# Optimization experiments

Measured on AMD Instinct MI355X. Metric: run time of the kernel, lower is better.

The kernel has to match this reference:

```python
import jax, jax.numpy as jnp
import numpy as np
import math

N = 50000      # nodes (single node type 'mapping_var')
D = 128        # in_feats
R = 3          # relations
E = 800000     # edges per relation
OUT = 64
ALPHA = 0.5
BETA1 = math.log(2.0)    # log(lambda/layer + 1), layer=1, lambda=1
BETA2 = math.log(1.5)    # layer=2
SLOPE = 0.01             # leaky_relu default negative slope


def setup_inputs() -> dict:
    key = jax.random.key(0)
    ks = jax.random.split(key, 8)
    x = jax.random.normal(ks[0], (N, D), dtype=jnp.float32)
    src = jax.random.randint(ks[1], (R, E), 0, N, dtype=jnp.int32)
    dst = jax.random.randint(ks[2], (R, E), 0, N, dtype=jnp.int32)
    W1 = jax.random.normal(ks[3], (R, D, D), dtype=jnp.float32) * 0.05
    b1 = jnp.zeros((R, D), dtype=jnp.float32)
    W2 = jax.random.normal(ks[4], (R, D, D), dtype=jnp.float32) * 0.05
    b2 = jnp.zeros((R, D), dtype=jnp.float32)
    Wlin = jax.random.normal(ks[5], (D, OUT), dtype=jnp.float32) * 0.05
    blin = jnp.zeros((OUT,), dtype=jnp.float32)
    return {"x": x, "src": src, "dst": dst, "W1": W1, "b1": b1,
            "W2": W2, "b2": b2, "Wlin": Wlin, "blin": blin}


def _gcn2_rel(h, feat0, src, dst, W, b, beta, act):
    """One GCN2Conv on one relation. h,feat0: [N,D]; src,dst: [E]."""
    ones = jnp.ones(src.shape, h.dtype)
    deg_out = jnp.maximum(jax.ops.segment_sum(ones, src, num_segments=N), 1.0)
    deg_in = jnp.maximum(jax.ops.segment_sum(ones, dst, num_segments=N), 1.0)
    hs = h * (deg_out ** -0.5)[:, None]              # src-side normalize
    agg = jax.ops.segment_sum(hs[src], dst, num_segments=N)  # SpMM via gather+scatter
    feat = agg * (deg_in ** -0.5)[:, None]           # dst-side normalize
    rst = feat * (1.0 - ALPHA) + ALPHA * feat0       # initial-residual blend
    rst = (1.0 - beta) * rst + beta * (rst @ W) + b  # identity mapping (project_initial_features)
    if act:
        rst = jnp.where(rst >= 0, rst, SLOPE * rst)  # leaky_relu
    return rst


def reference(x, src, dst, W1, b1, W2, b2, Wlin, blin):
    # conv1: per-relation GCN2Conv(layer=1, leaky_relu), mean-aggregate over relations
    h1 = jax.vmap(lambda s, d, w, bb: _gcn2_rel(x, x, s, d, w, bb, BETA1, True))(
        src, dst, W1, b1).mean(axis=0)
    # dropout: eval-mode identity
    # conv2: per-relation GCN2Conv(layer=2, no activation), feat_0 = original inputs
    h2 = jax.vmap(lambda s, d, w, bb: _gcn2_rel(h1, x, s, d, w, bb, BETA2, False))(
        src, dst, W2, b2).mean(axis=0)
    return h2 @ Wlin + blin
```

## Files before the change

### kernel.cpp

```cpp
#include <hip/hip_runtime.h>

#define NN    50000
#define DD    128
#define RR    3
#define EE    800000
#define OUTD  64
#define BKT   128
#define NBK   391
#define CAP   2560
#define CAPB  2560
#define CHUNK 2048
#define NCH   391
#define NPB   3125
#define SETUPB 6250
#define ALPHA_ 0.5f
#define SLOPE_ 0.01f
#define BETA1_ 0.6931471805599453f
#define BETA2_ 0.4054651081081644f

typedef __attribute__((ext_vector_type(8))) short short8;
typedef __attribute__((ext_vector_type(4))) float f32x4;

__device__ __forceinline__ unsigned short f2b(float f) {
    unsigned int u = __builtin_bit_cast(unsigned int, f);
    u += 0x7FFFu + ((u >> 16) & 1u);
    return (unsigned short)(u >> 16);
}
__device__ __forceinline__ unsigned int pack2(float lo, float hi) {
    return (unsigned int)f2b(lo) | ((unsigned int)f2b(hi) << 16);
}
__device__ __forceinline__ float blo(unsigned int w) { return __builtin_bit_cast(float, w << 16); }
__device__ __forceinline__ float bhi(unsigned int w) { return __builtin_bit_cast(float, w & 0xFFFF0000u); }

__global__ __launch_bounds__(256) void bin_kernel(
    const int* __restrict__ src, const int* __restrict__ dst,
    int* __restrict__ bcnt_d, int* __restrict__ bcnt_s,
    int* __restrict__ pairs_d, unsigned short* __restrict__ pairs_s)
{
    __shared__ int hist[NBK];
    __shared__ int lbase[NBK];
    __shared__ int gdelta[NBK];
    __shared__ int lcur[NBK];
    __shared__ unsigned int staging[CHUNK];
    unsigned short* staging16 = (unsigned short*)staging;
    const int tid = threadIdx.x;
    const int blk = blockIdx.x;
    const int phase = (blk >= RR * NCH);
    const int rb = phase ? blk - RR * NCH : blk;
    const int r = rb / NCH;
    const int chunk = rb % NCH;
    const int e0 = chunk * CHUNK;
    const int n = min(CHUNK, EE - e0);
    const int* sp = src + (size_t)r * EE + e0;
    const int* dp = dst + (size_t)r * EE + e0;
    const int* kp = phase ? sp : dp;

    for (int i = tid; i < NBK; i += 256) hist[i] = 0;
    __syncthreads();
    for (int i = tid; i < n; i += 256)
        atomicAdd(&hist[kp[i] >> 7], 1);
    __syncthreads();
    if (tid < 64) {
        int carry = 0;
        for (int c0 = 0; c0 < NBK; c0 += 64) {
            const int idx = c0 + tid;
            const int v = (idx < NBK) ? hist[idx] : 0;
            int incl = v;
            #pragma unroll
            for (int d = 1; d < 64; d <<= 1) {
                const int t = __shfl_up(incl, d, 64);
                if (tid >= d) incl += t;
            }
            if (idx < NBK) lbase[idx] = carry + incl - v;
            carry += __shfl(incl, 63, 64);
        }
    }
    __syncthreads();
    if (!phase) {
        for (int b = tid; b < NBK; b += 256) {
            lcur[b] = lbase[b];
            const int h = hist[b];
            if (h > 0) {
                const int gstart = (r * NBK + b) * CAP + atomicAdd(&bcnt_d[r * NBK + b], h);
                gdelta[b] = gstart - lbase[b];
            }
        }
        __syncthreads();
        for (int i = tid; i < n; i += 256) {
            const int d = dp[i];
            const int b = d >> 7;
            const int pos = atomicAdd(&lcur[b], 1);
            staging[pos] = (unsigned int)sp[i] | ((unsigned int)(d & 127) << 16)
                         | ((unsigned int)b << 23);
        }
        __syncthreads();
        for (int j = tid; j < n; j += 256) {
            const unsigned int v = staging[j];
            const int b = v >> 23;
            const int gi = gdelta[b] + j;
            const int lo = gi - (r * NBK + b) * CAP;
            if (lo < CAP) pairs_d[gi] = (int)(v & 0x7FFFFF);
        }
    } else {
        for (int b = tid; b < NBK; b += 256) {
            lcur[b] = lbase[b];
            const int h = hist[b];
            if (h > 0) {
                const int gstart = (r * NBK + b) * CAPB + atomicAdd(&bcnt_s[r * NBK + b], h);
                gdelta[b] = gstart - lbase[b];
            }
        }
        __syncthreads();
        for (int i = tid; i < n; i += 256) {
            const int s = sp[i];
            const int b = s >> 7;
            const int pos = atomicAdd(&lcur[b], 1);
            staging16[pos] = (unsigned short)((b << 7) | (s & 127));
        }
        __syncthreads();
        for (int j = tid; j < n; j += 256) {
            const unsigned short v = staging16[j];
            const int b = v >> 7;
            const int gi = gdelta[b] + j;
            const int lo = gi - (r * NBK + b) * CAPB;
            if (lo < CAPB) pairs_s[gi] = v;
        }
    }
}

__global__ __launch_bounds__(256) void dego_setup_kernel(
    const unsigned short* __restrict__ pairs_s, const int* __restrict__ bcnt_s,
    float* __restrict__ dego_r,
    const float* __restrict__ x, unsigned short* __restrict__ xb,
    const float* __restrict__ W1, const float* __restrict__ W2,
    const float* __restrict__ Wlin, unsigned short* __restrict__ Wt1,
    unsigned short* __restrict__ Wt2, unsigned short* __restrict__ WlT)
{
    __shared__ int scnt[BKT];
    const int tid = threadIdx.x;
    const int blk = blockIdx.x;
    if (blk < RR * NBK) {
        const int n2 = min(bcnt_s[blk], CAPB);
        const unsigned short* ps = pairs_s + (size_t)blk * CAPB;
        if (tid < BKT) scnt[tid] = 0;
        __syncthreads();
        for (int i = tid; i < n2; i += 256)
            atomicAdd(&scnt[ps[i] & 127], 1);
        __syncthreads();
        if (tid < BKT) {
            const int r = blk / NBK;
            const int g = (blk % NBK) * BKT + tid;
            if (g < NN)
                dego_r[r * NN + g] = rsqrtf((float)max(scnt[tid], 1));
        }
    } else {
        const int i = (blk - RR * NBK) * 256 + tid;
        {
            const float4 v = ((const float4*)x)[i];
            ushort4 o;
            o.x = f2b(v.x); o.y = f2b(v.y); o.z = f2b(v.z); o.w = f2b(v.w);
            ((ushort4*)xb)[i] = o;
        }
        if (i < RR * DD * DD) {
            const int r = i >> 14, rem = i & 16383, nn = rem >> 7, k = rem & 127;
            const float diag = (k == nn) ? 1.0f : 0.0f;
            const float w1 = W1[r * DD * DD + k * DD + nn];
            Wt1[i] = f2b(BETA1_ * w1 + diag * (1.0f - BETA1_));
            const float w2 = W2[r * DD * DD + k * DD + nn];
            Wt2[i] = f2b((BETA2_ * w2 + diag * (1.0f - BETA2_)) * (1.0f / 3.0f));
        } else if (i < RR * DD * DD + OUTD * DD) {
            const int j = i - RR * DD * DD;
            const int nn = j >> 7, k = j & 127;
            WlT[j] = f2b(Wlin[k * OUTD + nn]);
        }
    }
}

__global__ __launch_bounds__(256) void sort_kernel(
    int* __restrict__ pairs_d, const int* __restrict__ bcnt_d,
    const float* __restrict__ dego_r,
    int* __restrict__ off_g, int* __restrict__ cnt_g, float* __restrict__ degi_r)
{
    __shared__ int stage[CAP];
    __shared__ int cnt[BKT];
    __shared__ int base[BKT];
    __shared__ int pos[BKT];
    const int tid = threadIdx.x;
    const int bid = blockIdx.x;
    const int rr = bid / NBK;
    const int n = min(bcnt_d[bid], CAP);
    int* pp = pairs_d + (size_t)bid * CAP;
    const float* dego = dego_r + (size_t)rr * NN;
    if (tid < BKT) cnt[tid] = 0;
    __syncthreads();
    for (int i = tid; i < n; i += 256) {
        const int p = pp[i];
        stage[i] = p;
        atomicAdd(&cnt[p >> 16], 1);
    }
    __syncthreads();
    if (tid < 64) {
        int carry = 0;
        for (int c0 = 0; c0 < BKT; c0 += 64) {
            const int v = cnt[c0 + tid];
            int incl = v;
            #pragma unroll
            for (int d = 1; d < 64; d <<= 1) {
                const int t = __shfl_up(incl, d, 64);
                if (tid >= d) incl += t;
            }
            base[c0 + tid] = carry + incl - v;
            carry += __shfl(incl, 63, 64);
        }
    }
    __syncthreads();
    if (tid < BKT) {
        pos[tid] = base[tid];
        const int g = (bid % NBK) * BKT + tid;
        if (g < NN) {
            off_g[rr * NN + g] = bid * CAP + base[tid];
            cnt_g[rr * NN + g] = cnt[tid];
            degi_r[rr * NN + g] = rsqrtf((float)max(cnt[tid], 1));
        }
    }
    __syncthreads();
    for (int i = tid; i < n; i += 256) {
        const int p = stage[i];
        const int q = atomicAdd(&pos[p >> 16], 1);
        const int s = p & 0xFFFF;
        pp[q] = s | ((int)f2b(dego[s]) << 16);
    }
}

__global__ __launch_bounds__(256) void pull_all_kernel(
    const unsigned short* __restrict__ hb,
    const unsigned short* __restrict__ xb,
    const int* __restrict__ csrw, const int* __restrict__ off_g,
    const int* __restrict__ cnt_g, const float* __restrict__ degi_r,
    unsigned short* __restrict__ aggb)
{
    const int blk = blockIdx.x;
    const int r = blk / NPB;
    const int node = (blk % NPB) * 16 + (threadIdx.x >> 4);
    const int lane = threadIdx.x & 15;
    const int gi = r * NN + node;
    const int j0 = off_g[gi];
    const int j1 = j0 + cnt_g[gi];
    const uint4* hb4 = (const uint4*)hb;
    float a0 = 0.f, a1 = 0.f, a2 = 0.f, a3 = 0.f, a4 = 0.f, a5 = 0.f, a6 = 0.f, a7 = 0.f;
    int j = j0;
    for (; j + 4 <= j1; j += 4) {
        const unsigned int p0 = csrw[j],     p1 = csrw[j + 1];
        const unsigned int p2 = csrw[j + 2], p3 = csrw[j + 3];
        const float n0 = bhi(p0), n1 = bhi(p1), n2 = bhi(p2), n3 = bhi(p3);
        const uint4 q0 = hb4[(size_t)(p0 & 0xFFFF) * 16 + lane];
        const uint4 q1 = hb4[(size_t)(p1 & 0xFFFF) * 16 + lane];
        const uint4 q2 = hb4[(size_t)(p2 & 0xFFFF) * 16 + lane];
        const uint4 q3 = hb4[(size_t)(p3 & 0xFFFF) * 16 + lane];
        a0 += blo(q0.x) * n0 + blo(q1.x) * n1 + blo(q2.x) * n2 + blo(q3.x) * n3;
        a1 += bhi(q0.x) * n0 + bhi(q1.x) * n1 + bhi(q2.x) * n2 + bhi(q3.x) * n3;
        a2 += blo(q0.y) * n0 + blo(q1.y) * n1 + blo(q2.y) * n2 + blo(q3.y) * n3;
        a3 += bhi(q0.y) * n0 + bhi(q1.y) * n1 + bhi(q2.y) * n2 + bhi(q3.y) * n3;
        a4 += blo(q0.z) * n0 + blo(q1.z) * n1 + blo(q2.z) * n2 + blo(q3.z) * n3;
        a5 += bhi(q0.z) * n0 + bhi(q1.z) * n1 + bhi(q2.z) * n2 + bhi(q3.z) * n3;
        a6 += blo(q0.w) * n0 + blo(q1.w) * n1 + blo(q2.w) * n2 + blo(q3.w) * n3;
        a7 += bhi(q0.w) * n0 + bhi(q1.w) * n1 + bhi(q2.w) * n2 + bhi(q3.w) * n3;
    }
    for (; j < j1; ++j) {
        const unsigned int p0 = csrw[j];
        const float n0 = bhi(p0);
        const uint4 q0 = hb4[(size_t)(p0 & 0xFFFF) * 16 + lane];
        a0 += blo(q0.x) * n0; a1 += bhi(q0.x) * n0;
        a2 += blo(q0.y) * n0; a3 += bhi(q0.y) * n0;
        a4 += blo(q0.z) * n0; a5 += bhi(q0.z) * n0;
        a6 += blo(q0.w) * n0; a7 += bhi(q0.w) * n0;
    }
    const float nd = degi_r[gi] * (1.0f - ALPHA_);
    const uint4 xq = ((const uint4*)xb)[(size_t)node * 16 + lane];
    uint4 o;
    o.x = pack2(a0 * nd + ALPHA_ * blo(xq.x), a1 * nd + ALPHA_ * bhi(xq.x));
    o.y = pack2(a2 * nd + ALPHA_ * blo(xq.y), a3 * nd + ALPHA_ * bhi(xq.y));
    o.z = pack2(a4 * nd + ALPHA_ * blo(xq.z), a5 * nd + ALPHA_ * bhi(xq.z));
    o.w = pack2(a6 * nd + ALPHA_ * blo(xq.w), a7 * nd + ALPHA_ * bhi(xq.w));
    ((uint4*)aggb)[(size_t)gi * 16 + lane] = o;
}

template<int LIN>
__global__ __launch_bounds__(256) void conv_mfma_kernel(
    const unsigned short* __restrict__ aggb,
    const unsigned short* __restrict__ WtG,
    const float* __restrict__ bias,
    const unsigned short* __restrict__ WlT,
    const float* __restrict__ blin,
    unsigned short* __restrict__ houtb,
    float* __restrict__ outf)
{
    __shared__ unsigned short WtL[DD * 136];
    uint4* WtL4 = (uint4*)WtL;
    const int tid  = threadIdx.x;
    const int wave = tid >> 6;
    const int lane = tid & 63;
    const int l15  = lane & 15;
    const int q    = lane >> 4;
    const int blockRow = blockIdx.x * 64;
    const int row0 = blockRow + wave * 16;
    const int arow = min(row0 + l15, NN - 1);

    f32x4 o[8];
    if (LIN) {
        #pragma unroll
        for (int ct = 0; ct < 8; ++ct) {
            const int col = ct * 16 + l15;
            const float bv = (bias[col] + bias[DD + col] + bias[2 * DD + col]) * (1.0f / 3.0f);
            o[ct] = (f32x4){bv, bv, bv, bv};
        }
    } else {
        #pragma unroll
        for (int ct = 0; ct < 8; ++ct) o[ct] = (f32x4){0.f, 0.f, 0.f, 0.f};
    }

    for (int r = 0; r < RR; ++r) {
        __syncthreads();
        const uint4* wg = (const uint4*)(WtG + (size_t)r * DD * DD);
        for (int i = tid; i < DD * 16; i += 256)
            WtL4[(i >> 4) * 17 + (i & 15)] = wg[i];
        __syncthreads();

        short8 a[4];
        const uint4* ap = (const uint4*)aggb + ((size_t)r * NN + arow) * 16 + q;
        #pragma unroll
        for (int ks = 0; ks < 4; ++ks)
            a[ks] = __builtin_bit_cast(short8, ap[ks * 4]);

        #pragma unroll
        for (int ct = 0; ct < 8; ++ct) {
            f32x4 acc;
            if (LIN) {
                acc = o[ct];
            } else {
                const float bv = bias[r * DD + ct * 16 + l15];
                acc = (f32x4){bv, bv, bv, bv};
            }
            const int nrow = ct * 16 + l15;
            #pragma unroll
            for (int ks = 0; ks < 4; ++ks) {
                const short8 b = __builtin_bit_cast(short8, WtL4[nrow * 17 + ks * 4 + q]);
                acc = __builtin_amdgcn_mfma_f32_16x16x32_bf16(a[ks], b, acc, 0, 0, 0);
            }
            if (LIN) {
                o[ct] = acc;
            } else {
                #pragma unroll
                for (int e = 0; e < 4; ++e) {
                    float v = acc[e];
                    v = v >= 0.f ? v : SLOPE_ * v;
                    o[ct][e] += v * (1.0f / 3.0f);
                }
            }
        }
    }

    __syncthreads();
    unsigned short* tile = WtL;
    #pragma unroll
    for (int ct = 0; ct < 8; ++ct) {
        const int col = ct * 16 + l15;
        #pragma unroll
        for (int e = 0; e < 4; ++e) {
            const int lrow = wave * 16 + q * 4 + e;
            tile[lrow * 136 + col] = f2b(o[ct][e]);
        }
    }
    if (LIN) {
        uint4* wl4 = WtL4 + 64 * 17;
        const uint4* wg = (const uint4*)WlT;
        for (int i = tid; i < OUTD * 16; i += 256)
            wl4[(i >> 4) * 17 + (i & 15)] = wg[i];
    }
    __syncthreads();

    if (!LIN) {
        for (int i = tid; i < 64 * 16; i += 256) {
            const int lrow = i >> 4, c = i & 15;
            const int grow = blockRow + lrow;
            if (grow < NN)
                ((uint4*)houtb)[(size_t)grow * 16 + c] = WtL4[lrow * 17 + c];
        }
    } else {
        short8 a2[4];
        const int lrow = wave * 16 + l15;
        #pragma unroll
        for (int ks = 0; ks < 4; ++ks)
            a2[ks] = __builtin_bit_cast(short8, WtL4[lrow * 17 + ks * 4 + q]);
        #pragma unroll
        for (int ct = 0; ct < 4; ++ct) {
            const int col = ct * 16 + l15;
            const float bv = blin[col];
            f32x4 acc = (f32x4){bv, bv, bv, bv};
            #pragma unroll
            for (int ks = 0; ks < 4; ++ks) {
                const short8 b = __builtin_bit_cast(short8, WtL4[(64 + col) * 17 + ks * 4 + q]);
                acc = __builtin_amdgcn_mfma_f32_16x16x32_bf16(a2[ks], b, acc, 0, 0, 0);
            }
            #pragma unroll
            for (int e = 0; e < 4; ++e) {
                const int grow = row0 + q * 4 + e;
                if (grow < NN) outf[(size_t)grow * OUTD + col] = acc[e];
            }
        }
    }
}

extern "C" void kernel_launch(void* const* d_in, const int* in_sizes, int n_in,
                              void* d_out, int out_size, void* d_ws, size_t ws_size,
                              hipStream_t stream)
{
    const float* x    = (const float*)d_in[0];
    const int*   src  = (const int*)  d_in[1];
    const int*   dst  = (const int*)  d_in[2];
    const float* W1   = (const float*)d_in[3];
    const float* b1   = (const float*)d_in[4];
    const float* W2   = (const float*)d_in[5];
    const float* b2   = (const float*)d_in[6];
    const float* Wlin = (const float*)d_in[7];
    const float* blin = (const float*)d_in[8];
    float* out = (float*)d_out;

    int*   bcnt_d  = (int*)d_ws;
    int*   bcnt_s  = bcnt_d + RR * NBK;
    float* dego_r  = (float*)(bcnt_s + RR * NBK);
    float* degi_r  = dego_r + RR * NN;
    int*   off_g   = (int*)(degi_r + RR * NN);
    int*   cnt_g   = off_g + RR * NN;
    int*   pairs_d = cnt_g + RR * NN + 2;
    unsigned short* pairs_s = (unsigned short*)(pairs_d + (size_t)RR * NBK * CAP);
    unsigned short* xb   = pairs_s + (size_t)RR * NBK * CAPB;
    unsigned short* h1b  = xb + (size_t)NN * DD;
    unsigned short* aggb = h1b + (size_t)NN * DD;
    unsigned short* Wt1  = aggb + (size_t)RR * NN * DD;
    unsigned short* Wt2  = Wt1 + RR * DD * DD;
    unsigned short* WlT  = Wt2 + RR * DD * DD;

    hipMemsetAsync(bcnt_d, 0, (size_t)2 * RR * NBK * sizeof(int), stream);

    const int gemm_blocks = (NN + 63) / 64;

    bin_kernel<<<2 * RR * NCH, 256, 0, stream>>>(src, dst, bcnt_d, bcnt_s, pairs_d, pairs_s);
    dego_setup_kernel<<<RR * NBK + SETUPB, 256, 0, stream>>>(
        pairs_s, bcnt_s, dego_r, x, xb, W1, W2, Wlin, Wt1, Wt2, WlT);
    sort_kernel<<<RR * NBK, 256, 0, stream>>>(
        pairs_d, bcnt_d, dego_r, off_g, cnt_g, degi_r);

    pull_all_kernel<<<RR * NPB, 256, 0, stream>>>(
        xb, xb, pairs_d, off_g, cnt_g, degi_r, aggb);
    conv_mfma_kernel<0><<<gemm_blocks, 256, 0, stream>>>(
        aggb, Wt1, b1, nullptr, nullptr, h1b, nullptr);

    pull_all_kernel<<<RR * NPB, 256, 0, stream>>>(
        h1b, xb, pairs_d, off_g, cnt_g, degi_r, aggb);
    conv_mfma_kernel<1><<<gemm_blocks, 256, 0, stream>>>(
        aggb, Wt2, b2, WlT, blin, nullptr, out);
}
```

Before: 415.5 us.

## Fuse neighbor gather-aggregation into the MFMA conv kernel, eliminating the aggb intermediate

Replaces the separate pull (SpMM gather) kernel and the MFMA GEMM kernel with one fused kernel. Each lane gathers its 64-byte slice of neighbor rows and applies the degree scaling and residual blend in registers, then packs the result straight into MFMA A fragments. This removes the write and re-read of the 3×N×D bf16 aggregation buffer and two kernel launches per layer. In exchange, the irregular gather runs with far fewer threads: 782 blocks, 4 lanes per row, and relations processed one after another. That may expose memory latency and lower occupancy for what was a latency-bound gather.

New measurement: 457.9 us. 10.2% more time.

```diff
diff --git a/kernel.cpp b/kernel.cpp
--- a/kernel.cpp
+++ b/kernel.cpp
@@ -11,7 +11,6 @@
 #define CAPB  2560
 #define CHUNK 2048
 #define NCH   391
-#define NPB   3125
 #define SETUPB 6250
 #define ALPHA_ 0.5f
 #define SLOPE_ 0.01f
@@ -232,62 +231,12 @@
     }
 }
 
-__global__ __launch_bounds__(256) void pull_all_kernel(
+template<int LIN>
+__global__ __launch_bounds__(256, 4) void fused_conv_kernel(
     const unsigned short* __restrict__ hb,
     const unsigned short* __restrict__ xb,
     const int* __restrict__ csrw, const int* __restrict__ off_g,
     const int* __restrict__ cnt_g, const float* __restrict__ degi_r,
-    unsigned short* __restrict__ aggb)
-{
-    const int blk = blockIdx.x;
-    const int r = blk / NPB;
-    const int node = (blk % NPB) * 16 + (threadIdx.x >> 4);
-    const int lane = threadIdx.x & 15;
-    const int gi = r * NN + node;
-    const int j0 = off_g[gi];
-    const int j1 = j0 + cnt_g[gi];
-    const uint4* hb4 = (const uint4*)hb;
-    float a0 = 0.f, a1 = 0.f, a2 = 0.f, a3 = 0.f, a4 = 0.f, a5 = 0.f, a6 = 0.f, a7 = 0.f;
-    int j = j0;
-    for (; j + 4 <= j1; j += 4) {
-        const unsigned int p0 = csrw[j],     p1 = csrw[j + 1];
-        const unsigned int p2 = csrw[j + 2], p3 = csrw[j + 3];
-        const float n0 = bhi(p0), n1 = bhi(p1), n2 = bhi(p2), n3 = bhi(p3);
-        const uint4 q0 = hb4[(size_t)(p0 & 0xFFFF) * 16 + lane];
-        const uint4 q1 = hb4[(size_t)(p1 & 0xFFFF) * 16 + lane];
-        const uint4 q2 = hb4[(size_t)(p2 & 0xFFFF) * 16 + lane];
-        const uint4 q3 = hb4[(size_t)(p3 & 0xFFFF) * 16 + lane];
-        a0 += blo(q0.x) * n0 + blo(q1.x) * n1 + blo(q2.x) * n2 + blo(q3.x) * n3;
-        a1 += bhi(q0.x) * n0 + bhi(q1.x) * n1 + bhi(q2.x) * n2 + bhi(q3.x) * n3;
-        a2 += blo(q0.y) * n0 + blo(q1.y) * n1 + blo(q2.y) * n2 + blo(q3.y) * n3;
-        a3 += bhi(q0.y) * n0 + bhi(q1.y) * n1 + bhi(q2.y) * n2 + bhi(q3.y) * n3;
-        a4 += blo(q0.z) * n0 + blo(q1.z) * n1 + blo(q2.z) * n2 + blo(q3.z) * n3;
-        a5 += bhi(q0.z) * n0 + bhi(q1.z) * n1 + bhi(q2.z) * n2 + bhi(q3.z) * n3;
-        a6 += blo(q0.w) * n0 + blo(q1.w) * n1 + blo(q2.w) * n2 + blo(q3.w) * n3;
-        a7 += bhi(q0.w) * n0 + bhi(q1.w) * n1 + bhi(q2.w) * n2 + bhi(q3.w) * n3;
-    }
-    for (; j < j1; ++j) {
-        const unsigned int p0 = csrw[j];
-        const float n0 = bhi(p0);
-        const uint4 q0 = hb4[(size_t)(p0 & 0xFFFF) * 16 + lane];
-        a0 += blo(q0.x) * n0; a1 += bhi(q0.x) * n0;
-        a2 += blo(q0.y) * n0; a3 += bhi(q0.y) * n0;
-        a4 += blo(q0.z) * n0; a5 += bhi(q0.z) * n0;
-        a6 += blo(q0.w) * n0; a7 += bhi(q0.w) * n0;
-    }
-    const float nd = degi_r[gi] * (1.0f - ALPHA_);
-    const uint4 xq = ((const uint4*)xb)[(size_t)node * 16 + lane];
-    uint4 o;
-    o.x = pack2(a0 * nd + ALPHA_ * blo(xq.x), a1 * nd + ALPHA_ * bhi(xq.x));
-    o.y = pack2(a2 * nd + ALPHA_ * blo(xq.y), a3 * nd + ALPHA_ * bhi(xq.y));
-    o.z = pack2(a4 * nd + ALPHA_ * blo(xq.z), a5 * nd + ALPHA_ * bhi(xq.z));
-    o.w = pack2(a6 * nd + ALPHA_ * blo(xq.w), a7 * nd + ALPHA_ * bhi(xq.w));
-    ((uint4*)aggb)[(size_t)gi * 16 + lane] = o;
-}
-
-template<int LIN>
-__global__ __launch_bounds__(256) void conv_mfma_kernel(
-    const unsigned short* __restrict__ aggb,
     const unsigned short* __restrict__ WtG,
     const float* __restrict__ bias,
     const unsigned short* __restrict__ WlT,
@@ -306,6 +255,9 @@
     const int row0 = blockRow + wave * 16;
     const int arow = min(row0 + l15, NN - 1);
 
+    const uint4* hb4 = (const uint4*)hb;
+    const uint4* xb4 = (const uint4*)xb;
+
     f32x4 o[8];
     if (LIN) {
         #pragma unroll
@@ -324,35 +276,92 @@
         const uint4* wg = (const uint4*)(WtG + (size_t)r * DD * DD);
         for (int i = tid; i < DD * 16; i += 256)
             WtL4[(i >> 4) * 17 + (i & 15)] = wg[i];
-        __syncthreads();
-
+
+        const int gi = r * NN + arow;
+        const int j0 = off_g[gi];
+        const int j1 = j0 + cnt_g[gi];
+        float acc[4][8];
+        #pragma unroll
+        for (int ks = 0; ks < 4; ++ks)
+            #pragma unroll
+            for (int e = 0; e < 8; ++e) acc[ks][e] = 0.f;
+
+        int j = j0;
+        for (; j + 2 <= j1; j += 2) {
+            const unsigned int p0 = csrw[j], p1 = csrw[j + 1];
+            const float n0 = bhi(p0), n1 = bhi(p1);
+            const uint4* r0p = hb4 + (size_t)(p0 & 0xFFFF) * 16 + q;
+            const uint4* r1p = hb4 + (size_t)(p1 & 0xFFFF) * 16 + q;
+            uint4 u0[4], u1[4];
+            #pragma unroll
+            for (int ks = 0; ks < 4; ++ks) { u0[ks] = r0p[ks * 4]; u1[ks] = r1p[ks * 4]; }
+            #pragma unroll
+            for (int ks = 0; ks < 4; ++ks) {
+                acc[ks][0] += blo(u0[ks].x) * n0 + blo(u1[ks].x) * n1;
+                acc[ks][1] += bhi(u0[ks].x) * n0 + bhi(u1[ks].x) * n1;
+                acc[ks][2] += blo(u0[ks].y) * n0 + blo(u1[ks].y) * n1;
+                acc[ks][3] += bhi(u0[ks].y) * n0 + bhi(u1[ks].y) * n1;
+                acc[ks][4] += blo(u0[ks].z) * n0 + blo(u1[ks].z) * n1;
+                acc[ks][5] += bhi(u0[ks].z) * n0 + bhi(u1[ks].z) * n1;
+                acc[ks][6] += blo(u0[ks].w) * n0 + blo(u1[ks].w) * n1;
+                acc[ks][7] += bhi(u0[ks].w) * n0 + bhi(u1[ks].w) * n1;
+            }
+        }
+        if (j < j1) {
+            const unsigned int p0 = csrw[j];
+            const float n0 = bhi(p0);
+            const uint4* r0p = hb4 + (size_t)(p0 & 0xFFFF) * 16 + q;
+            uint4 u0[4];
+            #pragma unroll
+            for (int ks = 0; ks < 4; ++ks) u0[ks] = r0p[ks * 4];
+            #pragma unroll
+            for (int ks = 0; ks < 4; ++ks) {
+                acc[ks][0] += blo(u0[ks].x) * n0;
+                acc[ks][1] += bhi(u0[ks].x) * n0;
+                acc[ks][2] += blo(u0[ks].y) * n0;
+                acc[ks][3] += bhi(u0[ks].y) * n0;
+                acc[ks][4] += blo(u0[ks].z) * n0;
+                acc[ks][5] += bhi(u0[ks].z) * n0;
+                acc[ks][6] += blo(u0[ks].w) * n0;
+                acc[ks][7] += bhi(u0[ks].w) * n0;
+            }
+        }
+
+        const float nd = degi_r[gi] * (1.0f - ALPHA_);
         short8 a[4];
-        const uint4* ap = (const uint4*)aggb + ((size_t)r * NN + arow) * 16 + q;
-        #pragma unroll
-        for (int ks = 0; ks < 4; ++ks)
-            a[ks] = __builtin_bit_cast(short8, ap[ks * 4]);
+        #pragma unroll
+        for (int ks = 0; ks < 4; ++ks) {
+            const uint4 xq = xb4[(size_t)arow * 16 + ks * 4 + q];
+            uint4 pa;
+            pa.x = pack2(acc[ks][0] * nd + ALPHA_ * blo(xq.x), acc[ks][1] * nd + ALPHA_ * bhi(xq.x));
+            pa.y = pack2(acc[ks][2] * nd + ALPHA_ * blo(xq.y), acc[ks][3] * nd + ALPHA_ * bhi(xq.y));
+            pa.z = pack2(acc[ks][4] * nd + ALPHA_ * blo(xq.z), acc[ks][5] * nd + ALPHA_ * bhi(xq.z));
+            pa.w = pack2(acc[ks][6] * nd + ALPHA_ * blo(xq.w), acc[ks][7] * nd + ALPHA_ * bhi(xq.w));
+            a[ks] = __builtin_bit_cast(short8, pa);
+        }
+        __syncthreads();
 
         #pragma unroll
         for (int ct = 0; ct < 8; ++ct) {
-            f32x4 acc;
+            f32x4 acc2;
             if (LIN) {
-                acc = o[ct];
+                acc2 = o[ct];
             } else {
                 const float bv = bias[r * DD + ct * 16 + l15];
-                acc = (f32x4){bv, bv, bv, bv};
+                acc2 = (f32x4){bv, bv, bv, bv};
             }
             const int nrow = ct * 16 + l15;
             #pragma unroll
             for (int ks = 0; ks < 4; ++ks) {
                 const short8 b = __builtin_bit_cast(short8, WtL4[nrow * 17 + ks * 4 + q]);
-                acc = __builtin_amdgcn_mfma_f32_16x16x32_bf16(a[ks], b, acc, 0, 0, 0);
+                acc2 = __builtin_amdgcn_mfma_f32_16x16x32_bf16(a[ks], b, acc2, 0, 0, 0);
             }
             if (LIN) {
-                o[ct] = acc;
+                o[ct] = acc2;
             } else {
                 #pragma unroll
                 for (int e = 0; e < 4; ++e) {
-                    float v = acc[e];
+                    float v = acc2[e];
                     v = v >= 0.f ? v : SLOPE_ * v;
                     o[ct][e] += v * (1.0f / 3.0f);
                 }
@@ -451,13 +460,9 @@
     sort_kernel<<<RR * NBK, 256, 0, stream>>>(
         pairs_d, bcnt_d, dego_r, off_g, cnt_g, degi_r);
 
-    pull_all_kernel<<<RR * NPB, 256, 0, stream>>>(
-        xb, xb, pairs_d, off_g, cnt_g, degi_r, aggb);
-    conv_mfma_kernel<0><<<gemm_blocks, 256, 0, stream>>>(
-        aggb, Wt1, b1, nullptr, nullptr, h1b, nullptr);
-
-    pull_all_kernel<<<RR * NPB, 256, 0, stream>>>(
-        h1b, xb, pairs_d, off_g, cnt_g, degi_r, aggb);
-    conv_mfma_kernel<1><<<gemm_blocks, 256, 0, stream>>>(
-        aggb, Wt2, b2, WlT, blin, nullptr, out);
-}
+    fused_conv_kernel<0><<<gemm_blocks, 256, 0, stream>>>(
+        xb, xb, pairs_d, off_g, cnt_g, degi_r, Wt1, b1, nullptr, nullptr, h1b, nullptr);
+
+    fused_conv_kernel<1><<<gemm_blocks, 256, 0, stream>>>(
+        h1b, xb, pairs_d, off_g, cnt_g, degi_r, Wt2, b2, WlT, blin, nullptr, out);
+}
```

## Replace source-side binning with global atomic out-degree count and fuse prep kernels

Applied to the files above, without the earlier changes.

Drops the second binning pass over src edges and the separate kernel that counted out-degree per bucket. Out-degrees are now counted with direct global atomics on an int array, and the dst binning, degree counting and weight/feature conversion all run in one launch. The rsqrt of out-degree moves into the sort kernel. It also doubles the chunk size for dst binning. This saves one kernel launch and the pairs_s traffic, in exchange for 2.4M scattered global atomics and a larger memset.

Result: slower. 469.4 us (+13.0%).

```diff
diff --git a/kernel.cpp b/kernel.cpp
--- a/kernel.cpp
+++ b/kernel.cpp
@@ -8,10 +8,10 @@
 #define BKT   128
 #define NBK   391
 #define CAP   2560
-#define CAPB  2560
-#define CHUNK 2048
-#define NCH   391
+#define CHUNK 4096
+#define NCH   196
 #define NPB   3125
+#define EDGEB 2344
 #define SETUPB 6250
 #define ALPHA_ 0.5f
 #define SLOPE_ 0.01f
@@ -32,51 +32,52 @@
 __device__ __forceinline__ float blo(unsigned int w) { return __builtin_bit_cast(float, w << 16); }
 __device__ __forceinline__ float bhi(unsigned int w) { return __builtin_bit_cast(float, w & 0xFFFF0000u); }
 
-__global__ __launch_bounds__(256) void bin_kernel(
+__global__ __launch_bounds__(256) void prep_kernel(
     const int* __restrict__ src, const int* __restrict__ dst,
-    int* __restrict__ bcnt_d, int* __restrict__ bcnt_s,
-    int* __restrict__ pairs_d, unsigned short* __restrict__ pairs_s)
+    int* __restrict__ bcnt_d, int* __restrict__ pairs_d,
+    int* __restrict__ dego_cnt,
+    const float* __restrict__ x, unsigned short* __restrict__ xb,
+    const float* __restrict__ W1, const float* __restrict__ W2,
+    const float* __restrict__ Wlin, unsigned short* __restrict__ Wt1,
+    unsigned short* __restrict__ Wt2, unsigned short* __restrict__ WlT)
 {
     __shared__ int hist[NBK];
     __shared__ int lbase[NBK];
     __shared__ int gdelta[NBK];
     __shared__ int lcur[NBK];
     __shared__ unsigned int staging[CHUNK];
-    unsigned short* staging16 = (unsigned short*)staging;
     const int tid = threadIdx.x;
     const int blk = blockIdx.x;
-    const int phase = (blk >= RR * NCH);
-    const int rb = phase ? blk - RR * NCH : blk;
-    const int r = rb / NCH;
-    const int chunk = rb % NCH;
-    const int e0 = chunk * CHUNK;
-    const int n = min(CHUNK, EE - e0);
-    const int* sp = src + (size_t)r * EE + e0;
-    const int* dp = dst + (size_t)r * EE + e0;
-    const int* kp = phase ? sp : dp;
-
-    for (int i = tid; i < NBK; i += 256) hist[i] = 0;
-    __syncthreads();
-    for (int i = tid; i < n; i += 256)
-        atomicAdd(&hist[kp[i] >> 7], 1);
-    __syncthreads();
-    if (tid < 64) {
-        int carry = 0;
-        for (int c0 = 0; c0 < NBK; c0 += 64) {
-            const int idx = c0 + tid;
-            const int v = (idx < NBK) ? hist[idx] : 0;
-            int incl = v;
-            #pragma unroll
-            for (int d = 1; d < 64; d <<= 1) {
-                const int t = __shfl_up(incl, d, 64);
-                if (tid >= d) incl += t;
-            }
-            if (idx < NBK) lbase[idx] = carry + incl - v;
-            carry += __shfl(incl, 63, 64);
-        }
-    }
-    __syncthreads();
-    if (!phase) {
+
+    if (blk < RR * NCH) {
+        const int r = blk / NCH;
+        const int chunk = blk % NCH;
+        const int e0 = chunk * CHUNK;
+        const int n = min(CHUNK, EE - e0);
+        const int* sp = src + (size_t)r * EE + e0;
+        const int* dp = dst + (size_t)r * EE + e0;
+
+        for (int i = tid; i < NBK; i += 256) hist[i] = 0;
+        __syncthreads();
+        for (int i = tid; i < n; i += 256)
+            atomicAdd(&hist[dp[i] >> 7], 1);
+        __syncthreads();
+        if (tid < 64) {
+            int carry = 0;
+            for (int c0 = 0; c0 < NBK; c0 += 64) {
+                const int idx = c0 + tid;
+                const int v = (idx < NBK) ? hist[idx] : 0;
+                int incl = v;
+                #pragma unroll
+                for (int d = 1; d < 64; d <<= 1) {
+                    const int t = __shfl_up(incl, d, 64);
+                    if (tid >= d) incl += t;
+                }
+                if (idx < NBK) lbase[idx] = carry + incl - v;
+                carry += __shfl(incl, 63, 64);
+            }
+        }
+        __syncthreads();
         for (int b = tid; b < NBK; b += 256) {
             lcur[b] = lbase[b];
             const int h = hist[b];
@@ -101,60 +102,20 @@
             const int lo = gi - (r * NBK + b) * CAP;
             if (lo < CAP) pairs_d[gi] = (int)(v & 0x7FFFFF);
         }
+    } else if (blk < RR * NCH + EDGEB) {
+        const int base = (blk - RR * NCH) * 1024 + tid;
+        #pragma unroll
+        for (int k = 0; k < 4; ++k) {
+            const int e = base + k * 256;
+            if (e < RR * EE) {
+                int r = 0;
+                if (e >= EE) r = 1;
+                if (e >= 2 * EE) r = 2;
+                atomicAdd(&dego_cnt[r * NN + src[e]], 1);
+            }
+        }
     } else {
-        for (int b = tid; b < NBK; b += 256) {
-            lcur[b] = lbase[b];
-            const int h = hist[b];
-            if (h > 0) {
-                const int gstart = (r * NBK + b) * CAPB + atomicAdd(&bcnt_s[r * NBK + b], h);
-                gdelta[b] = gstart - lbase[b];
-            }
-        }
-        __syncthreads();
-        for (int i = tid; i < n; i += 256) {
-            const int s = sp[i];
-            const int b = s >> 7;
-            const int pos = atomicAdd(&lcur[b], 1);
-            staging16[pos] = (unsigned short)((b << 7) | (s & 127));
-        }
-        __syncthreads();
-        for (int j = tid; j < n; j += 256) {
-            const unsigned short v = staging16[j];
-            const int b = v >> 7;
-            const int gi = gdelta[b] + j;
-            const int lo = gi - (r * NBK + b) * CAPB;
-            if (lo < CAPB) pairs_s[gi] = v;
-        }
-    }
-}
-
-__global__ __launch_bounds__(256) void dego_setup_kernel(
-    const unsigned short* __restrict__ pairs_s, const int* __restrict__ bcnt_s,
-    float* __restrict__ dego_r,
-    const float* __restrict__ x, unsigned short* __restrict__ xb,
-    const float* __restrict__ W1, const float* __restrict__ W2,
-    const float* __restrict__ Wlin, unsigned short* __restrict__ Wt1,
-    unsigned short* __restrict__ Wt2, unsigned short* __restrict__ WlT)
-{
-    __shared__ int scnt[BKT];
-    const int tid = threadIdx.x;
-    const int blk = blockIdx.x;
-    if (blk < RR * NBK) {
-        const int n2 = min(bcnt_s[blk], CAPB);
-        const unsigned short* ps = pairs_s + (size_t)blk * CAPB;
-        if (tid < BKT) scnt[tid] = 0;
-        __syncthreads();
-        for (int i = tid; i < n2; i += 256)
-            atomicAdd(&scnt[ps[i] & 127], 1);
-        __syncthreads();
-        if (tid < BKT) {
-            const int r = blk / NBK;
-            const int g = (blk % NBK) * BKT + tid;
-            if (g < NN)
-                dego_r[r * NN + g] = rsqrtf((float)max(scnt[tid], 1));
-        }
-    } else {
-        const int i = (blk - RR * NBK) * 256 + tid;
+        const int i = (blk - RR * NCH - EDGEB) * 256 + tid;
         {
             const float4 v = ((const float4*)x)[i];
             ushort4 o;
@@ -178,7 +139,7 @@
 
 __global__ __launch_bounds__(256) void sort_kernel(
     int* __restrict__ pairs_d, const int* __restrict__ bcnt_d,
-    const float* __restrict__ dego_r,
+    const int* __restrict__ dego_cnt,
     int* __restrict__ off_g, int* __restrict__ cnt_g, float* __restrict__ degi_r)
 {
     __shared__ int stage[CAP];
@@ -190,7 +151,7 @@
     const int rr = bid / NBK;
     const int n = min(bcnt_d[bid], CAP);
     int* pp = pairs_d + (size_t)bid * CAP;
-    const float* dego = dego_r + (size_t)rr * NN;
+    const int* dego = dego_cnt + (size_t)rr * NN;
     if (tid < BKT) cnt[tid] = 0;
     __syncthreads();
     for (int i = tid; i < n; i += 256) {
@@ -228,7 +189,8 @@
         const int p = stage[i];
         const int q = atomicAdd(&pos[p >> 16], 1);
         const int s = p & 0xFFFF;
-        pp[q] = s | ((int)f2b(dego[s]) << 16);
+        const int dv = dego[s];
+        pp[q] = s | ((int)f2b(rsqrtf((float)max(dv, 1))) << 16);
     }
 }
 
@@ -426,30 +388,27 @@
     const float* blin = (const float*)d_in[8];
     float* out = (float*)d_out;
 
-    int*   bcnt_d  = (int*)d_ws;
-    int*   bcnt_s  = bcnt_d + RR * NBK;
-    float* dego_r  = (float*)(bcnt_s + RR * NBK);
-    float* degi_r  = dego_r + RR * NN;
-    int*   off_g   = (int*)(degi_r + RR * NN);
-    int*   cnt_g   = off_g + RR * NN;
-    int*   pairs_d = cnt_g + RR * NN + 2;
-    unsigned short* pairs_s = (unsigned short*)(pairs_d + (size_t)RR * NBK * CAP);
-    unsigned short* xb   = pairs_s + (size_t)RR * NBK * CAPB;
+    int*   bcnt_d   = (int*)d_ws;
+    int*   dego_cnt = bcnt_d + RR * NBK;
+    float* degi_r   = (float*)(dego_cnt + RR * NN);
+    int*   off_g    = (int*)(degi_r + RR * NN);
+    int*   cnt_g    = off_g + RR * NN;
+    int*   pairs_d  = cnt_g + RR * NN + 3;
+    unsigned short* xb   = (unsigned short*)(pairs_d + (size_t)RR * NBK * CAP);
     unsigned short* h1b  = xb + (size_t)NN * DD;
     unsigned short* aggb = h1b + (size_t)NN * DD;
     unsigned short* Wt1  = aggb + (size_t)RR * NN * DD;
     unsigned short* Wt2  = Wt1 + RR * DD * DD;
     unsigned short* WlT  = Wt2 + RR * DD * DD;
 
-    hipMemsetAsync(bcnt_d, 0, (size_t)2 * RR * NBK * sizeof(int), stream);
+    hipMemsetAsync(bcnt_d, 0, (size_t)(RR * NBK + RR * NN) * sizeof(int), stream);
 
     const int gemm_blocks = (NN + 63) / 64;
 
-    bin_kernel<<<2 * RR * NCH, 256, 0, stream>>>(src, dst, bcnt_d, bcnt_s, pairs_d, pairs_s);
-    dego_setup_kernel<<<RR * NBK + SETUPB, 256, 0, stream>>>(
-        pairs_s, bcnt_s, dego_r, x, xb, W1, W2, Wlin, Wt1, Wt2, WlT);
+    prep_kernel<<<RR * NCH + EDGEB + SETUPB, 256, 0, stream>>>(
+        src, dst, bcnt_d, pairs_d, dego_cnt, x, xb, W1, W2, Wlin, Wt1, Wt2, WlT);
     sort_kernel<<<RR * NBK, 256, 0, stream>>>(
-        pairs_d, bcnt_d, dego_r, off_g, cnt_g, degi_r);
+        pairs_d, bcnt_d, dego_cnt, off_g, cnt_g, degi_r);
 
     pull_all_kernel<<<RR * NPB, 256, 0, stream>>>(
         xb, xb, pairs_d, off_g, cnt_g, degi_r, aggb);
```

## Split SpMM gather into feature-column passes over degree-sorted node permutation

Applied to the files above, without the earlier changes.

Adds a degree histogram in the sort kernel and a new perm kernel that orders nodes by in-degree per relation. The pull kernel becomes four launches per layer, each handling a 32-column slice with 4 lanes per node, visiting nodes in degree order. The aim is a smaller gather working set per pass for better L2 hit rates and more balanced wave work. It also software-prefetches the next relation's A tile in the MFMA conv kernel. In exchange it adds extra kernel launches, re-reads of the CSR indices in every pass, and narrower 16-lane-wide gathers.

New measurement: 923.1 us. +122.2%, slower.

```diff
diff --git a/kernel.cpp b/kernel.cpp
--- a/kernel.cpp
+++ b/kernel.cpp
@@ -11,7 +11,7 @@
 #define CAPB  2560
 #define CHUNK 2048
 #define NCH   391
-#define NPB   3125
+#define NB64  782
 #define SETUPB 6250
 #define ALPHA_ 0.5f
 #define SLOPE_ 0.01f
@@ -179,7 +179,8 @@
 __global__ __launch_bounds__(256) void sort_kernel(
     int* __restrict__ pairs_d, const int* __restrict__ bcnt_d,
     const float* __restrict__ dego_r,
-    int* __restrict__ off_g, int* __restrict__ cnt_g, float* __restrict__ degi_r)
+    int* __restrict__ off_g, int* __restrict__ cnt_g, float* __restrict__ degi_r,
+    int* __restrict__ deghist)
 {
     __shared__ int stage[CAP];
     __shared__ int cnt[BKT];
@@ -221,6 +222,7 @@
             off_g[rr * NN + g] = bid * CAP + base[tid];
             cnt_g[rr * NN + g] = cnt[tid];
             degi_r[rr * NN + g] = rsqrtf((float)max(cnt[tid], 1));
+            atomicAdd(&deghist[rr * 64 + min(cnt[tid], 63)], 1);
         }
     }
     __syncthreads();
@@ -232,31 +234,71 @@
     }
 }
 
-__global__ __launch_bounds__(256) void pull_all_kernel(
+__global__ __launch_bounds__(128) void perm_kernel(
+    const int* __restrict__ cnt_g, const int* __restrict__ deghist,
+    int* __restrict__ degcur, int* __restrict__ perm)
+{
+    __shared__ int lcnt[64];
+    __shared__ int lbase[64];
+    __shared__ int pre[64];
+    const int tid = threadIdx.x;
+    const int bid = blockIdx.x;
+    const int rr = bid / NBK;
+    if (tid < 64) {
+        lcnt[tid] = 0;
+        const int h = deghist[rr * 64 + tid];
+        int incl = h;
+        #pragma unroll
+        for (int d = 1; d < 64; d <<= 1) {
+            const int t = __shfl_up(incl, d, 64);
+            if (tid >= d) incl += t;
+        }
+        pre[tid] = incl - h;
+    }
+    __syncthreads();
+    const int g = (bid % NBK) * BKT + tid;
+    const bool valid = (g < NN);
+    int deg = 0, lrank = 0;
+    if (valid) {
+        deg = min(cnt_g[rr * NN + g], 63);
+        lrank = atomicAdd(&lcnt[deg], 1);
+    }
+    __syncthreads();
+    if (tid < 64 && lcnt[tid] > 0)
+        lbase[tid] = atomicAdd(&degcur[rr * 64 + tid], lcnt[tid]);
+    __syncthreads();
+    if (valid)
+        perm[rr * NN + pre[deg] + lbase[deg] + lrank] = g;
+}
+
+__global__ __launch_bounds__(256) void pull_pass_kernel(
     const unsigned short* __restrict__ hb,
     const unsigned short* __restrict__ xb,
     const int* __restrict__ csrw, const int* __restrict__ off_g,
     const int* __restrict__ cnt_g, const float* __restrict__ degi_r,
-    unsigned short* __restrict__ aggb)
+    const int* __restrict__ perm,
+    unsigned short* __restrict__ aggb, const int pass)
 {
     const int blk = blockIdx.x;
-    const int r = blk / NPB;
-    const int node = (blk % NPB) * 16 + (threadIdx.x >> 4);
-    const int lane = threadIdx.x & 15;
+    const int r = blk / NB64;
+    const int nidx = (blk % NB64) * 64 + (threadIdx.x >> 2);
+    const int lane4 = threadIdx.x & 3;
+    if (nidx >= NN) return;
+    const int node = perm[r * NN + nidx];
     const int gi = r * NN + node;
     const int j0 = off_g[gi];
     const int j1 = j0 + cnt_g[gi];
-    const uint4* hb4 = (const uint4*)hb;
+    const uint4* hb4 = (const uint4*)hb + pass * 4 + lane4;
     float a0 = 0.f, a1 = 0.f, a2 = 0.f, a3 = 0.f, a4 = 0.f, a5 = 0.f, a6 = 0.f, a7 = 0.f;
     int j = j0;
     for (; j + 4 <= j1; j += 4) {
         const unsigned int p0 = csrw[j],     p1 = csrw[j + 1];
         const unsigned int p2 = csrw[j + 2], p3 = csrw[j + 3];
         const float n0 = bhi(p0), n1 = bhi(p1), n2 = bhi(p2), n3 = bhi(p3);
-        const uint4 q0 = hb4[(size_t)(p0 & 0xFFFF) * 16 + lane];
-        const uint4 q1 = hb4[(size_t)(p1 & 0xFFFF) * 16 + lane];
-        const uint4 q2 = hb4[(size_t)(p2 & 0xFFFF) * 16 + lane];
-        const uint4 q3 = hb4[(size_t)(p3 & 0xFFFF) * 16 + lane];
+        const uint4 q0 = hb4[(size_t)(p0 & 0xFFFF) * 16];
+        const uint4 q1 = hb4[(size_t)(p1 & 0xFFFF) * 16];
+        const uint4 q2 = hb4[(size_t)(p2 & 0xFFFF) * 16];
+        const uint4 q3 = hb4[(size_t)(p3 & 0xFFFF) * 16];
         a0 += blo(q0.x) * n0 + blo(q1.x) * n1 + blo(q2.x) * n2 + blo(q3.x) * n3;
         a1 += bhi(q0.x) * n0 + bhi(q1.x) * n1 + bhi(q2.x) * n2 + bhi(q3.x) * n3;
         a2 += blo(q0.y) * n0 + blo(q1.y) * n1 + blo(q2.y) * n2 + blo(q3.y) * n3;
@@ -269,20 +311,20 @@
     for (; j < j1; ++j) {
         const unsigned int p0 = csrw[j];
         const float n0 = bhi(p0);
-        const uint4 q0 = hb4[(size_t)(p0 & 0xFFFF) * 16 + lane];
+        const uint4 q0 = hb4[(size_t)(p0 & 0xFFFF) * 16];
         a0 += blo(q0.x) * n0; a1 += bhi(q0.x) * n0;
         a2 += blo(q0.y) * n0; a3 += bhi(q0.y) * n0;
         a4 += blo(q0.z) * n0; a5 += bhi(q0.z) * n0;
         a6 += blo(q0.w) * n0; a7 += bhi(q0.w) * n0;
     }
     const float nd = degi_r[gi] * (1.0f - ALPHA_);
-    const uint4 xq = ((const uint4*)xb)[(size_t)node * 16 + lane];
+    const uint4 xq = ((const uint4*)xb)[(size_t)node * 16 + pass * 4 + lane4];
     uint4 o;
     o.x = pack2(a0 * nd + ALPHA_ * blo(xq.x), a1 * nd + ALPHA_ * bhi(xq.x));
     o.y = pack2(a2 * nd + ALPHA_ * blo(xq.y), a3 * nd + ALPHA_ * bhi(xq.y));
     o.z = pack2(a4 * nd + ALPHA_ * blo(xq.z), a5 * nd + ALPHA_ * bhi(xq.z));
     o.w = pack2(a6 * nd + ALPHA_ * blo(xq.w), a7 * nd + ALPHA_ * bhi(xq.w));
-    ((uint4*)aggb)[(size_t)gi * 16 + lane] = o;
+    ((uint4*)aggb)[(size_t)gi * 16 + pass * 4 + lane4] = o;
 }
 
 template<int LIN>
@@ -319,18 +361,26 @@
         for (int ct = 0; ct < 8; ++ct) o[ct] = (f32x4){0.f, 0.f, 0.f, 0.f};
     }
 
+    short8 a_cur[4], a_nxt[4];
+    {
+        const uint4* ap = (const uint4*)aggb + (size_t)arow * 16 + q;
+        #pragma unroll
+        for (int ks = 0; ks < 4; ++ks)
+            a_cur[ks] = __builtin_bit_cast(short8, ap[ks * 4]);
+    }
+
     for (int r = 0; r < RR; ++r) {
         __syncthreads();
         const uint4* wg = (const uint4*)(WtG + (size_t)r * DD * DD);
         for (int i = tid; i < DD * 16; i += 256)
             WtL4[(i >> 4) * 17 + (i & 15)] = wg[i];
-        __syncthreads();
-
-        short8 a[4];
-        const uint4* ap = (const uint4*)aggb + ((size_t)r * NN + arow) * 16 + q;
-        #pragma unroll
-        for (int ks = 0; ks < 4; ++ks)
-            a[ks] = __builtin_bit_cast(short8, ap[ks * 4]);
+        if (r + 1 < RR) {
+            const uint4* ap = (const uint4*)aggb + ((size_t)(r + 1) * NN + arow) * 16 + q;
+            #pragma unroll
+            for (int ks = 0; ks < 4; ++ks)
+                a_nxt[ks] = __builtin_bit_cast(short8, ap[ks * 4]);
+        }
+        __syncthreads();
 
         #pragma unroll
         for (int ct = 0; ct < 8; ++ct) {
@@ -345,7 +395,7 @@
             #pragma unroll
             for (int ks = 0; ks < 4; ++ks) {
                 const short8 b = __builtin_bit_cast(short8, WtL4[nrow * 17 + ks * 4 + q]);
-                acc = __builtin_amdgcn_mfma_f32_16x16x32_bf16(a[ks], b, acc, 0, 0, 0);
+                acc = __builtin_amdgcn_mfma_f32_16x16x32_bf16(a_cur[ks], b, acc, 0, 0, 0);
             }
             if (LIN) {
                 o[ct] = acc;
@@ -358,6 +408,8 @@
                 }
             }
         }
+        #pragma unroll
+        for (int ks = 0; ks < 4; ++ks) a_cur[ks] = a_nxt[ks];
     }
 
     __syncthreads();
@@ -428,12 +480,15 @@
 
     int*   bcnt_d  = (int*)d_ws;
     int*   bcnt_s  = bcnt_d + RR * NBK;
-    float* dego_r  = (float*)(bcnt_s + RR * NBK);
+    int*   deghist = bcnt_s + RR * NBK;
+    int*   degcur  = deghist + RR * 64;
+    float* dego_r  = (float*)(degcur + RR * 64);
     float* degi_r  = dego_r + RR * NN;
     int*   off_g   = (int*)(degi_r + RR * NN);
     int*   cnt_g   = off_g + RR * NN;
     int*   pairs_d = cnt_g + RR * NN + 2;
     unsigned short* pairs_s = (unsigned short*)(pairs_d + (size_t)RR * NBK * CAP);
+    int*   perm    = (int*)pairs_s;
     unsigned short* xb   = pairs_s + (size_t)RR * NBK * CAPB;
     unsigned short* h1b  = xb + (size_t)NN * DD;
     unsigned short* aggb = h1b + (size_t)NN * DD;
@@ -441,7 +496,7 @@
     unsigned short* Wt2  = Wt1 + RR * DD * DD;
     unsigned short* WlT  = Wt2 + RR * DD * DD;
 
-    hipMemsetAsync(bcnt_d, 0, (size_t)2 * RR * NBK * sizeof(int), stream);
+    hipMemsetAsync(bcnt_d, 0, (size_t)(2 * RR * NBK + 2 * RR * 64) * sizeof(int), stream);
 
     const int gemm_blocks = (NN + 63) / 64;
 
@@ -449,15 +504,18 @@
     dego_setup_kernel<<<RR * NBK + SETUPB, 256, 0, stream>>>(
         pairs_s, bcnt_s, dego_r, x, xb, W1, W2, Wlin, Wt1, Wt2, WlT);
     sort_kernel<<<RR * NBK, 256, 0, stream>>>(
-        pairs_d, bcnt_d, dego_r, off_g, cnt_g, degi_r);
-
-    pull_all_kernel<<<RR * NPB, 256, 0, stream>>>(
-        xb, xb, pairs_d, off_g, cnt_g, degi_r, aggb);
+        pairs_d, bcnt_d, dego_r, off_g, cnt_g, degi_r, deghist);
+    perm_kernel<<<RR * NBK, 128, 0, stream>>>(cnt_g, deghist, degcur, perm);
+
+    for (int p = 0; p < 4; ++p)
+        pull_pass_kernel<<<RR * NB64, 256, 0, stream>>>(
+            xb, xb, pairs_d, off_g, cnt_g, degi_r, perm, aggb, p);
     conv_mfma_kernel<0><<<gemm_blocks, 256, 0, stream>>>(
         aggb, Wt1, b1, nullptr, nullptr, h1b, nullptr);
 
-    pull_all_kernel<<<RR * NPB, 256, 0, stream>>>(
-        h1b, xb, pairs_d, off_g, cnt_g, degi_r, aggb);
+    for (int p = 0; p < 4; ++p)
+        pull_pass_kernel<<<RR * NB64, 256, 0, stream>>>(
+            h1b, xb, pairs_d, off_g, cnt_g, degi_r, perm, aggb, p);
     conv_mfma_kernel<1><<<gemm_blocks, 256, 0, stream>>>(
         aggb, Wt2, b2, WlT, blin, nullptr, out);
 }
```
